# Performance work log

Hardware: AMD Instinct MI355X
Metric: run time of the kernel (lower is better)

The kernel has to match this reference:

```python
import jax, jax.numpy as jnp
import numpy as np

EMBED = 1024
HEADS = 16
HEAD_DIM = EMBED // HEADS


def setup_inputs() -> dict:
    key = jax.random.key(0)
    ks = jax.random.split(key, 9)
    s = 1.0 / np.sqrt(EMBED)
    return {
        "embeddings": jax.random.normal(ks[0], (4, 2048, EMBED), dtype=jnp.float32),
        "wq": jax.random.uniform(ks[1], (EMBED, EMBED), jnp.float32, -s, s),
        "bq": jax.random.uniform(ks[2], (EMBED,), jnp.float32, -s, s),
        "wk": jax.random.uniform(ks[3], (EMBED, EMBED), jnp.float32, -s, s),
        "bk": jax.random.uniform(ks[4], (EMBED,), jnp.float32, -s, s),
        "wv": jax.random.uniform(ks[5], (EMBED, EMBED), jnp.float32, -s, s),
        "bv": jax.random.uniform(ks[6], (EMBED,), jnp.float32, -s, s),
        "wo": jax.random.uniform(ks[7], (EMBED, EMBED), jnp.float32, -s, s),
        "bo": jax.random.uniform(ks[8], (EMBED,), jnp.float32, -s, s),
    }


def reference(embeddings, wq, bq, wk, bk, wv, bv, wo, bo):
    b, s, _ = embeddings.shape
    # Projections: x @ W^T + b (torch nn.Linear convention)
    q = (embeddings @ wq.T + bq).reshape(b, s, HEADS, HEAD_DIM)
    k = (embeddings @ wk.T + bk).reshape(b, s, HEADS, HEAD_DIM)
    v = (embeddings @ wv.T + bv).reshape(b, s, HEADS, HEAD_DIM)
    scale = 1.0 / np.sqrt(HEAD_DIM).astype(np.float32)
    # scores: [b, h, s, s]
    scores = jnp.einsum("bqhd,bkhd->bhqk", q, k) * scale
    probs = jax.nn.softmax(scores, axis=-1)
    attn = jnp.einsum("bhqk,bkhd->bqhd", probs, v).reshape(b, s, EMBED)
    return attn @ wo.T + bo
```

## Files before the change

### kernel.cpp

```cpp
#include <hip/hip_runtime.h>
#include <hip/hip_bf16.h>
#include <math.h>

using bf16x8 = __attribute__((ext_vector_type(8))) short;
using f32x4  = __attribute__((ext_vector_type(4))) float;
using f32x16 = __attribute__((ext_vector_type(16))) float;
using i32x4  = __attribute__((ext_vector_type(4))) int;

#define MFMA_BF16(a, b, c) __builtin_amdgcn_mfma_f32_16x16x32_bf16((a), (b), (c), 0, 0, 0)
#define MFMA32(a, b, c)    __builtin_amdgcn_mfma_f32_32x32x16_bf16((a), (b), (c), 0, 0, 0)

__device__ __forceinline__ float bf2f(short s) {
    union { unsigned u; float f; } v;
    v.u = ((unsigned)(unsigned short)s) << 16;
    return v.f;
}
__device__ __forceinline__ short f2bf(float f) {
    union { float f; unsigned u; } v; v.f = f;
    unsigned r = v.u + 0x7FFF + ((v.u >> 16) & 1);
    return (short)(r >> 16);
}
__device__ __forceinline__ int pack_bf16_rhu(float lo, float hi) {
    union { float f; unsigned u; } a, b; a.f = lo; b.f = hi;
    unsigned x = a.u + 0x8000u, y = b.u + 0x8000u;
#if __has_builtin(__builtin_amdgcn_perm)
    return (int)__builtin_amdgcn_perm(y, x, 0x07060302u);
#else
    return (int)((y & 0xFFFF0000u) | (x >> 16));
#endif
}
__device__ __forceinline__ int cvtpk_bf16(float lo, float hi) {
    int r;
    asm("v_cvt_pk_bf16_f32 %0, %1, %2" : "=v"(r) : "v"(lo), "v"(hi));
    return r;
}
__device__ __forceinline__ void permswap(int &a, int &b) {
#if __has_builtin(__builtin_amdgcn_permlane32_swap)
    typedef unsigned u32x2v __attribute__((ext_vector_type(2)));
    u32x2v r = __builtin_amdgcn_permlane32_swap((unsigned)a, (unsigned)b, false, false);
    a = (int)r[0]; b = (int)r[1];
#else
    asm volatile("v_permlane32_swap_b32 %0, %1" : "+v"(a), "+v"(b));
#endif
}
__device__ __forceinline__ float fexp2(float x) {
#if __has_builtin(__builtin_amdgcn_exp2f)
    return __builtin_amdgcn_exp2f(x);
#else
    return exp2f(x);
#endif
}

__device__ __forceinline__ void gload_lds16(const void* g, void* l) {
    __builtin_amdgcn_global_load_lds(
        (const __attribute__((address_space(1))) void*)g,
        (__attribute__((address_space(3))) void*)l, 16, 0, 0);
}

__global__ void detect_dtype(const unsigned short* __restrict__ emb, int* flag) {
    __shared__ int tot;
    if (threadIdx.x == 0) tot = 0;
    __syncthreads();
    int c = 0;
    for (int i = 0; i < 64; i++) {
        unsigned short v = emb[2 * (threadIdx.x * 64 + i)];
        unsigned e = (v >> 7) & 0xFF;
        if (v == 0 || v == 0x8000u || (e >= 97 && e <= 137)) c++;
    }
    atomicAdd(&tot, c);
    __syncthreads();
    if (threadIdx.x == 0) *flag = (tot > 8192) ? 1 : 0;
}

__global__ void convert8(const void* __restrict__ src, short* __restrict__ dst,
                         int n8, const int* __restrict__ flag) {
    int i = blockIdx.x * 256 + threadIdx.x;
    if (i >= n8) return;
    if (*flag) {
        ((bf16x8*)dst)[i] = ((const bf16x8*)src)[i];
    } else {
        const float* f = (const float*)src + (size_t)i * 8;
        bf16x8 o;
#pragma unroll
        for (int j = 0; j < 8; j++) o[j] = f2bf(f[j]);
        ((bf16x8*)dst)[i] = o;
    }
}

__global__ void convert_all(
    const void* __restrict__ w0, const void* __restrict__ w1,
    const void* __restrict__ w2, const void* __restrict__ w3,
    const void* __restrict__ b0, const void* __restrict__ b1,
    const void* __restrict__ b2, const void* __restrict__ b3,
    short* dw0, short* dw1, short* dw2, short* dw3,
    short* db0, short* db1, short* db2, short* db3,
    const int* __restrict__ flag)
{
    int i = blockIdx.x * 256 + threadIdx.x;
    const void* src; short* dst; int idx;
    if (i < 524288) {
        int w = i >> 17; idx = i & 131071;
        src = (w == 0) ? w0 : (w == 1) ? w1 : (w == 2) ? w2 : w3;
        dst = (w == 0) ? dw0 : (w == 1) ? dw1 : (w == 2) ? dw2 : dw3;
    } else {
        int j = i - 524288; int b = j >> 7; idx = j & 127;
        src = (b == 0) ? b0 : (b == 1) ? b1 : (b == 2) ? b2 : b3;
        dst = (b == 0) ? db0 : (b == 1) ? db1 : (b == 2) ? db2 : db3;
    }
    if (*flag) {
        ((bf16x8*)dst)[idx] = ((const bf16x8*)src)[idx];
    } else {
        const float* f = (const float*)src + (size_t)idx * 8;
        bf16x8 o;
#pragma unroll
        for (int j = 0; j < 8; j++) o[j] = f2bf(f[j]);
        ((bf16x8*)dst)[idx] = o;
    }
}

__global__ __launch_bounds__(256) void gemm128(
    const short* __restrict__ A,
    const short* __restrict__ B0, const short* __restrict__ B1,
    const short* __restrict__ B2,
    const short* __restrict__ bias0, const short* __restrict__ bias1,
    const short* __restrict__ bias2,
    void* __restrict__ C0, void* __restrict__ C1, void* __restrict__ C2,
    float s0, float s1, float s2,
    int mode0, int mode1, int mode2,
    const int* __restrict__ flag)
{
    constexpr int M = 8192, N = 1024, Kd = 1024, BK = 32;
    __shared__ __align__(16) short As[128 * BK];
    __shared__ __align__(16) short Bs[128 * BK];

    const int z = blockIdx.z;
    const short* B    = (z == 0) ? B0    : (z == 1) ? B1    : B2;
    const short* bias = (z == 0) ? bias0 : (z == 1) ? bias1 : bias2;
    void*  C     = (z == 0) ? C0 : (z == 1) ? C1 : C2;
    float  scale = (z == 0) ? s0 : (z == 1) ? s1 : s2;
    int    mode  = (z == 0) ? mode0 : (z == 1) ? mode1 : mode2;

    const int tid  = threadIdx.x;
    const int lane = tid & 63;
    const int wave = tid >> 6;
    const int lr   = lane & 15;
    const int quad = lane >> 4;
    const int q8   = quad * 8;

    const int m0 = (blockIdx.x >> 3) * 128;
    const int n0 = (blockIdx.x & 7) * 128;
    const int wm = (wave >> 1) * 64;
    const int wn = (wave & 1) * 64;

    const int srow = lane >> 2;
    const int scol = (lane & 3) * 8;

    int fl = 1;
    if (mode == 2) fl = *flag;

    f32x4 acc[4][4];
#pragma unroll
    for (int i = 0; i < 4; i++)
#pragma unroll
        for (int j = 0; j < 4; j++) acc[i][j] = (f32x4){0.f, 0.f, 0.f, 0.f};

    for (int k0 = 0; k0 < Kd; k0 += BK) {
#pragma unroll
        for (int t = 0; t < 2; t++) {
            const int r = wave * 32 + t * 16;
            gload_lds16(A + (size_t)(m0 + r + srow) * Kd + k0 + scol,
                        As + r * BK);
            gload_lds16(B + (size_t)(n0 + r + srow) * Kd + k0 + scol,
                        Bs + r * BK);
        }
        __syncthreads();

        bf16x8 a[4], b[4];
#pragma unroll
        for (int i = 0; i < 4; i++)
            a[i] = *(const bf16x8*)(As + (wm + i * 16 + lr) * BK + q8);
#pragma unroll
        for (int j = 0; j < 4; j++)
            b[j] = *(const bf16x8*)(Bs + (wn + j * 16 + lr) * BK + q8);
#pragma unroll
        for (int i = 0; i < 4; i++)
#pragma unroll
            for (int j = 0; j < 4; j++)
                acc[i][j] = MFMA_BF16(a[i], b[j], acc[i][j]);
        __syncthreads();
    }

#pragma unroll
    for (int j = 0; j < 4; j++) {
        const int col = n0 + wn + j * 16 + lr;
        const float bv = bf2f(bias[col]);
#pragma unroll
        for (int i = 0; i < 4; i++) {
#pragma unroll
            for (int r = 0; r < 4; r++) {
                const int row = m0 + wm + i * 16 + quad * 4 + r;
                const float v = (acc[i][j][r] + bv) * scale;
                if (mode == 1)      ((short*)C)[(size_t)col * M + row] = f2bf(v);
                else if (mode == 0) ((short*)C)[(size_t)row * N + col] = f2bf(v);
                else {
                    if (fl) ((short*)C)[(size_t)row * N + col] = f2bf(v);
                    else    ((float*)C)[(size_t)row * N + col] = v;
                }
            }
        }
    }
}

__global__ __launch_bounds__(256) void attn_kernel(
    const short* Q, const short* __restrict__ K,
    const short* __restrict__ Vt, short* Aout)
{
    __shared__ __align__(16) short lds[2][2][64][64];

    const int tid  = threadIdx.x;
    const int lane = tid & 63;
    const int wave = tid >> 6;
    const int l31  = lane & 31;
    const int hi   = lane >> 5;
    const int xr   = l31 & 7;

    const int qt = blockIdx.x;
    const int bh = blockIdx.y;
    const int b  = bh >> 4, h = bh & 15;
    const int q0 = b * 2048 + qt * 128 + wave * 32;
    const int c0 = h * 64;

    const int sr = lane >> 3;
    const int sc = ((lane & 7) ^ sr) * 8;
    const int sarr = wave >> 1;

    const short* Kb = K  + (size_t)(b * 2048) * 1024 + c0;
    const short* Vb = Vt + (size_t)c0 * 8192 + b * 2048;

    bf16x8 qf[4];
#pragma unroll
    for (int slot = 0; slot < 4; slot++)
        qf[slot] = *(const bf16x8*)(Q + (size_t)(q0 + l31) * 1024 + c0 + slot * 16 + hi * 8);

    auto stage = [&](int bufi, int kt) {
#pragma unroll
        for (int t = 0; t < 4; t++) {
            const int r0 = ((wave & 1) * 4 + t) * 8;
            short* dst = &lds[bufi][sarr][r0][0];
            if (sarr == 0)
                gload_lds16(Kb + (size_t)(kt + r0 + sr) * 1024 + sc, dst);
            else
                gload_lds16(Vb + (size_t)(r0 + sr) * 8192 + kt + sc, dst);
        }
    };

    float l_run = 0.f;
    f32x16 o[2];
#pragma unroll
    for (int dblk = 0; dblk < 2; dblk++)
#pragma unroll
        for (int r = 0; r < 16; r++) o[dblk][r] = 0.f;

    stage(0, 0);
    for (int kt = 0; kt < 2048; kt += 64) {
        const int cur = (kt >> 6) & 1;
        stage(cur ^ 1, (kt + 64) & 2047);
        asm volatile("s_waitcnt vmcnt(4)" ::: "memory");
        __builtin_amdgcn_s_barrier();
        __builtin_amdgcn_sched_barrier(0);

        f32x16 st[2];
#pragma unroll
        for (int blk = 0; blk < 2; blk++)
#pragma unroll
            for (int r = 0; r < 16; r++) st[blk][r] = 0.f;

#pragma unroll
        for (int blk = 0; blk < 2; blk++)
#pragma unroll
            for (int slot = 0; slot < 4; slot++) {
                bf16x8 kf = *(const bf16x8*)
                    &lds[cur][0][blk * 32 + l31][(((slot << 1) | hi) ^ xr) * 8];
                st[blk] = MFMA32(kf, qf[slot], st[blk]);
            }

        float rs = 0.f;
#pragma unroll
        for (int blk = 0; blk < 2; blk++)
#pragma unroll
            for (int r = 0; r < 16; r++) {
                float p = fexp2(st[blk][r]);
                st[blk][r] = p;
                rs += p;
            }
        l_run += rs;

#pragma unroll
        for (int ks = 0; ks < 4; ks++) {
            const int blk = ks >> 1;
            const int rb  = (ks & 1) * 8;
            int A0 = cvtpk_bf16(st[blk][rb + 0], st[blk][rb + 1]);
            int A1 = cvtpk_bf16(st[blk][rb + 2], st[blk][rb + 3]);
            int B0 = cvtpk_bf16(st[blk][rb + 4], st[blk][rb + 5]);
            int B1 = cvtpk_bf16(st[blk][rb + 6], st[blk][rb + 7]);
            permswap(A0, B0);
            permswap(A1, B1);
            i32x4 paw; paw[0] = A0; paw[1] = A1; paw[2] = B0; paw[3] = B1;
            const bf16x8 pf = *(const bf16x8*)&paw;
#pragma unroll
            for (int dblk = 0; dblk < 2; dblk++) {
                bf16x8 vf = *(const bf16x8*)
                    &lds[cur][1][dblk * 32 + l31][(((ks << 1) | hi) ^ xr) * 8];
                o[dblk] = MFMA32(pf, vf, o[dblk]);
            }
        }

        asm volatile("s_waitcnt lgkmcnt(0)" ::: "memory");
        __builtin_amdgcn_sched_barrier(0);
        __builtin_amdgcn_s_barrier();
    }

    float l_tot = l_run + __shfl_xor(l_run, 32);
#pragma unroll
    for (int r = 0; r < 16; r++) {
        const int qrow = (r & 3) + 8 * (r >> 2) + 4 * hi;
        const float inv = 1.f / __shfl(l_tot, qrow);
#pragma unroll
        for (int dblk = 0; dblk < 2; dblk++)
            Aout[(size_t)(q0 + qrow) * 1024 + c0 + dblk * 32 + l31] =
                f2bf(o[dblk][r] * inv);
    }
}

extern "C" void kernel_launch(void* const* d_in, const int* in_sizes, int n_in,
                              void* d_out, int out_size, void* d_ws, size_t ws_size,
                              hipStream_t stream)
{
    const size_t MB = (size_t)1024 * 1024;
    char* ws = (char*)d_ws;

    int*   flagp = (int*)ws;
    short* embC  = (short*)(ws + 1 * MB);
    short* wC[4] = { (short*)(ws + 17 * MB), (short*)(ws + 19 * MB),
                     (short*)(ws + 21 * MB), (short*)(ws + 23 * MB) };
    short* bC[4] = { (short*)(ws + 25 * MB), (short*)(ws + 25 * MB + 4096),
                     (short*)(ws + 25 * MB + 8192), (short*)(ws + 25 * MB + 12288) };

    short *Qb, *Kb, *Vt, *Ab;
    if (ws_size >= 90 * MB) {
        Qb = (short*)(ws + 26 * MB);
        Kb = (short*)(ws + 42 * MB);
        Vt = (short*)(ws + 58 * MB);
        Ab = (short*)(ws + 74 * MB);
    } else {
        Qb = (short*)(ws + 26 * MB);
        Kb = (short*)d_out;
        Vt = (short*)(ws + 42 * MB);
        Ab = Qb;
    }

    detect_dtype<<<1, 256, 0, stream>>>((const unsigned short*)d_in[0], flagp);

    convert8<<<4096, 256, 0, stream>>>(d_in[0], embC, 1048576, flagp);
    convert_all<<<2050, 256, 0, stream>>>(
        d_in[1], d_in[3], d_in[5], d_in[7],
        d_in[2], d_in[4], d_in[6], d_in[8],
        wC[0], wC[1], wC[2], wC[3],
        bC[0], bC[1], bC[2], bC[3], flagp);

    dim3 blk(256);
    gemm128<<<dim3(512, 1, 3), blk, 0, stream>>>(
        embC, wC[0], wC[1], wC[2], bC[0], bC[1], bC[2],
        Qb, Kb, Vt, 0.18033688011112042f, 1.0f, 1.0f, 0, 0, 1, nullptr);

    attn_kernel<<<dim3(16, 64), blk, 0, stream>>>(Qb, Kb, Vt, Ab);

    gemm128<<<dim3(512, 1, 1), blk, 0, stream>>>(
        Ab, wC[3], nullptr, nullptr, bC[3], nullptr, nullptr,
        d_out, nullptr, nullptr, 1.0f, 0.f, 0.f, 2, 0, 0, flagp);
}
```

Before: 330.3 us.

## Double-buffer LDS in projection GEMM, swizzle LDS chunks and block order

Turns the projection GEMM's shared-memory staging into a two-buffer pipeline. The next K tile is issued with direct global-to-LDS loads before the current tile is computed, using manual waitcnt and barriers in place of two __syncthreads per step. It also XOR-swizzles the 16-byte column chunks in LDS to reduce bank conflicts, and remaps block indices so blocks sharing the same B panel run together for better L2 reuse. The costs are double the LDS footprint and fragile hand-written wait counts: the last iteration issues a redundant wrapped-around load, and the vmcnt(4) value must match the number of loads in flight.

```diff
diff --git a/kernel.cpp b/kernel.cpp
--- a/kernel.cpp
+++ b/kernel.cpp
@@ -19,15 +19,6 @@
     union { float f; unsigned u; } v; v.f = f;
     unsigned r = v.u + 0x7FFF + ((v.u >> 16) & 1);
     return (short)(r >> 16);
-}
-__device__ __forceinline__ int pack_bf16_rhu(float lo, float hi) {
-    union { float f; unsigned u; } a, b; a.f = lo; b.f = hi;
-    unsigned x = a.u + 0x8000u, y = b.u + 0x8000u;
-#if __has_builtin(__builtin_amdgcn_perm)
-    return (int)__builtin_amdgcn_perm(y, x, 0x07060302u);
-#else
-    return (int)((y & 0xFFFF0000u) | (x >> 16));
-#endif
 }
 __device__ __forceinline__ int cvtpk_bf16(float lo, float hi) {
     int r;
@@ -130,8 +121,8 @@
     const int* __restrict__ flag)
 {
     constexpr int M = 8192, N = 1024, Kd = 1024, BK = 32;
-    __shared__ __align__(16) short As[128 * BK];
-    __shared__ __align__(16) short Bs[128 * BK];
+    __shared__ __align__(16) short As[2][128 * BK];
+    __shared__ __align__(16) short Bs[2][128 * BK];
 
     const int z = blockIdx.z;
     const short* B    = (z == 0) ? B0    : (z == 1) ? B1    : B2;
@@ -145,15 +136,17 @@
     const int wave = tid >> 6;
     const int lr   = lane & 15;
     const int quad = lane >> 4;
-    const int q8   = quad * 8;
-
-    const int m0 = (blockIdx.x >> 3) * 128;
-    const int n0 = (blockIdx.x & 7) * 128;
+
+    const int bid = blockIdx.x;
+    const int swz = ((bid & 7) << 6) | (bid >> 3);
+    const int m0 = (swz >> 3) * 128;
+    const int n0 = (swz & 7) * 128;
     const int wm = (wave >> 1) * 64;
     const int wn = (wave & 1) * 64;
 
     const int srow = lane >> 2;
-    const int scol = (lane & 3) * 8;
+    const int scol = (((lane & 3) ^ ((lane >> 3) & 3)) * 8);
+    const int rchunk = (quad ^ ((lr >> 1) & 3)) * 8;
 
     int fl = 1;
     if (mode == 2) fl = *flag;
@@ -164,30 +157,41 @@
 #pragma unroll
         for (int j = 0; j < 4; j++) acc[i][j] = (f32x4){0.f, 0.f, 0.f, 0.f};
 
-    for (int k0 = 0; k0 < Kd; k0 += BK) {
+    auto stage = [&](int bufi, int k) {
 #pragma unroll
         for (int t = 0; t < 2; t++) {
             const int r = wave * 32 + t * 16;
-            gload_lds16(A + (size_t)(m0 + r + srow) * Kd + k0 + scol,
-                        As + r * BK);
-            gload_lds16(B + (size_t)(n0 + r + srow) * Kd + k0 + scol,
-                        Bs + r * BK);
+            gload_lds16(A + (size_t)(m0 + r + srow) * Kd + k + scol,
+                        &As[bufi][r * BK]);
+            gload_lds16(B + (size_t)(n0 + r + srow) * Kd + k + scol,
+                        &Bs[bufi][r * BK]);
         }
-        __syncthreads();
+    };
+
+    stage(0, 0);
+    for (int k0 = 0; k0 < Kd; k0 += BK) {
+        const int cur = (k0 >> 5) & 1;
+        stage(cur ^ 1, (k0 + BK) & (Kd - 1));
+        asm volatile("s_waitcnt vmcnt(4)" ::: "memory");
+        __builtin_amdgcn_s_barrier();
+        __builtin_amdgcn_sched_barrier(0);
 
         bf16x8 a[4], b[4];
 #pragma unroll
         for (int i = 0; i < 4; i++)
-            a[i] = *(const bf16x8*)(As + (wm + i * 16 + lr) * BK + q8);
+            a[i] = *(const bf16x8*)(&As[cur][(wm + i * 16 + lr) * BK + rchunk]);
 #pragma unroll
         for (int j = 0; j < 4; j++)
-            b[j] = *(const bf16x8*)(Bs + (wn + j * 16 + lr) * BK + q8);
+            b[j] = *(const bf16x8*)(&Bs[cur][(wn + j * 16 + lr) * BK + rchunk]);
 #pragma unroll
         for (int i = 0; i < 4; i++)
 #pragma unroll
             for (int j = 0; j < 4; j++)
                 acc[i][j] = MFMA_BF16(a[i], b[j], acc[i][j]);
-        __syncthreads();
+
+        asm volatile("s_waitcnt lgkmcnt(0)" ::: "memory");
+        __builtin_amdgcn_sched_barrier(0);
+        __builtin_amdgcn_s_barrier();
     }
 
 #pragma unroll
```

New measurement: 325.0 us. Within noise of the previous version (-1.6%).
